# Performance work log

Hardware: AMD Instinct MI355X
Metric: run time of the kernel (lower is better)

Reference implementation:

```python
import jax, jax.numpy as jnp
import numpy as np

B, N, H, D = 2, 2048, 16, 128

def setup_inputs() -> dict:
    key = jax.random.key(0)
    kq, kk, kv = jax.random.split(key, 3)
    return {
        "query": jax.random.normal(kq, (B, N, H, D), dtype=jnp.float32),
        "key": jax.random.normal(kk, (B, N, H, D), dtype=jnp.float32),
        "value": jax.random.normal(kv, (B, N, H, D), dtype=jnp.float32),
    }

def reference(query, key, value):
    # inputs are [b, n, h, d]; module transposes to [b, h, n, d]
    q = jnp.transpose(query, (0, 2, 1, 3))  # bhnd
    k = jnp.transpose(key, (0, 2, 1, 3))    # bhmd
    v = jnp.transpose(value, (0, 2, 1, 3))  # bhmd
    # NOTE: original applies NO 1/sqrt(d) scaling
    scores = jnp.einsum('bhnd,bhmd->bhnm', q, k)
    attn = jax.nn.softmax(scores, axis=-1)
    return jnp.einsum('bhnm,bhmd->bhnd', attn, v)  # [b, h, n, d]
```

## Files before the change

kernel.cpp:

```cpp
#include <hip/hip_runtime.h>
#include <hip/hip_bf16.h>
#include <stdint.h>


constexpr int Bb = 2, Nn = 2048, Hh = 16, Dd = 128;
constexpr int ROWSTR = Hh * Dd;
constexpr size_t TEN_ELEMS = (size_t)Bb * Nn * Hh * Dd;
constexpr size_t WS_NEED = 3 * TEN_ELEMS * 2;

typedef __attribute__((ext_vector_type(8))) _Float16 f16x8;
typedef __attribute__((ext_vector_type(4))) float f32x4;

__device__ __forceinline__ unsigned short f2h(float f) {
  union { _Float16 h; unsigned short u; } v;
  v.h = (_Float16)f;
  return v.u;
}

__device__ __forceinline__ void gload_lds16(const void* g, void* l) {
  __builtin_amdgcn_global_load_lds(
      (const __attribute__((address_space(1))) unsigned int*)g,
      (__attribute__((address_space(3))) unsigned int*)l, 16, 0, 0);
}

__global__ __launch_bounds__(512) void conv_qk(
    const float* __restrict__ Q, const float* __restrict__ K,
    _Float16* __restrict__ Qf, _Float16* __restrict__ Kf) {
  size_t id = (size_t)blockIdx.x * 512 + threadIdx.x;
  const float* src;
  _Float16* dst;
  size_t e;
  if (id < TEN_ELEMS / 8) { src = Q; dst = Qf; e = id * 8; }
  else { src = K; dst = Kf; e = (id - TEN_ELEMS / 8) * 8; }
  float4 a = *(const float4*)(src + e);
  float4 b = *(const float4*)(src + e + 4);
  f16x8 t;
  t[0] = (_Float16)a.x; t[1] = (_Float16)a.y; t[2] = (_Float16)a.z; t[3] = (_Float16)a.w;
  t[4] = (_Float16)b.x; t[5] = (_Float16)b.y; t[6] = (_Float16)b.z; t[7] = (_Float16)b.w;
  *(f16x8*)(dst + e) = t;
}

__global__ __launch_bounds__(256) void conv_v(
    const float* __restrict__ V, _Float16* __restrict__ Vt) {
  __shared__ alignas(16) short T[128 * 72];
  const int tid = threadIdx.x;
  const int bid = blockIdx.x;
  const int bh = bid >> 5;
  const int n0 = (bid & 31) * 64;
  const int h = bh & 15, b = bh >> 4;
  const float* src = V + (((size_t)b * Nn + n0) * Hh + h) * Dd;
#pragma unroll
  for (int it = 0; it < 8; ++it) {
    int id = it * 256 + tid;
    int f = id & 31, n = id >> 5;
    float4 a = *(const float4*)(src + (size_t)n * ROWSTR + f * 4);
    T[(4 * f + 0) * 72 + n] = (short)f2h(a.x);
    T[(4 * f + 1) * 72 + n] = (short)f2h(a.y);
    T[(4 * f + 2) * 72 + n] = (short)f2h(a.z);
    T[(4 * f + 3) * 72 + n] = (short)f2h(a.w);
  }
  __syncthreads();
  _Float16* dst = Vt + (size_t)bh * Dd * Nn + n0;
#pragma unroll
  for (int it = 0; it < 4; ++it) {
    int cid = it * 256 + tid;
    int d = cid >> 3, nc = cid & 7;
    f16x8 v = *(const f16x8*)((const char*)T + d * 144 + nc * 16);
    *(f16x8*)(dst + (size_t)d * Nn + nc * 8) = v;
  }
}

__global__ __launch_bounds__(512, 2) void attn_f16(
    const _Float16* __restrict__ Qf, const _Float16* __restrict__ Kf,
    const _Float16* __restrict__ Vt, float* __restrict__ O) {
  __shared__ alignas(16) short LDS[98304 / 2];
  char* base = (char*)LDS;

  const int tid = threadIdx.x;
  const int wave = tid >> 6;
  const int lane = tid & 63;
  const int g = (lane >> 4) & 3;
  const int l15 = lane & 15;

  const int raw = blockIdx.x;
  const int wg = (raw & 7) * 32 + (raw >> 3);
  const int qb = wg & 7;
  const int bh = wg >> 3;
  const int h = bh & 15, b = bh >> 4;
  const int q0 = qb * 256;

  const char* K0 = (const char*)Kf + ((size_t)b * Nn * Hh + h) * 256;
  const char* Q0 = (const char*)Qf + ((size_t)b * Nn * Hh + h) * 256;
  const char* V0 = (const char*)Vt + (size_t)bh * Dd * Nn * 2;
  float* Ob = O + (size_t)bh * Nn * Dd;

  const int wq0 = q0 + wave * 32;
  f16x8 qf[2][4];
#pragma unroll
  for (int qs = 0; qs < 2; ++qs) {
    const char* qp = Q0 + (size_t)(wq0 + qs * 16 + l15) * 4096;
#pragma unroll
    for (int c = 0; c < 4; ++c)
      qf[qs][c] = *(const f16x8*)(qp + c * 64 + g * 16);
  }

  f32x4 acc[2][8];
#pragma unroll
  for (int qs = 0; qs < 2; ++qs)
#pragma unroll
    for (int dt = 0; dt < 8; ++dt) acc[qs][dt] = (f32x4){0.f, 0.f, 0.f, 0.f};
  float m_run[2][4], l_run[2][4];
#pragma unroll
  for (int qs = 0; qs < 2; ++qs)
#pragma unroll
    for (int r = 0; r < 4; ++r) { m_run[qs][r] = -INFINITY; l_run[qs][r] = 0.f; }

  char* PB = base + 65536 + wave * 4096;

  auto STAGE = [&](int bufsel, int kt) {
    const int kv0 = kt * 64;
    char* kdst = base + bufsel * 16384;
    char* vdst = base + 32768 + bufsel * 16384;
#pragma unroll
    for (int i = 0; i < 2; ++i) {
      int ob = i * 8192 + wave * 1024;
      int o = ob + lane * 16;
      int kv = o >> 8, ir = o & 255;
      gload_lds16(K0 + (size_t)(kv0 + kv) * 4096 + (ir ^ ((kv & 7) << 4)), kdst + ob);
      int d = o >> 7, ir2 = o & 127;
      gload_lds16(V0 + (size_t)d * 4096 + kv0 * 2 + (ir2 ^ ((d & 7) << 4)), vdst + ob);
    }
  };

  STAGE(0, 0);
  __syncthreads();
  int cur = 0;

  for (int kt = 0; kt < Nn / 64; ++kt) {
    if (kt < Nn / 64 - 1) STAGE(cur ^ 1, kt + 1);
    const char* KB = base + cur * 16384;
    const char* VB = base + 32768 + cur * 16384;

    f32x4 s[2][4];
#pragma unroll
    for (int qs = 0; qs < 2; ++qs)
#pragma unroll
      for (int t4 = 0; t4 < 4; ++t4) s[qs][t4] = (f32x4){0.f, 0.f, 0.f, 0.f};
#pragma unroll
    for (int t4 = 0; t4 < 4; ++t4) {
      const int row = t4 * 16 + l15;
      const int ro = row * 256;
      const int swz = (row & 7) << 4;
#pragma unroll
      for (int c = 0; c < 4; ++c) {
        f16x8 kf = *(const f16x8*)(KB + ro + ((c * 64 + g * 16) ^ swz));
        s[0][t4] = __builtin_amdgcn_mfma_f32_16x16x32_f16(qf[0][c], kf, s[0][t4], 0, 0, 0);
        s[1][t4] = __builtin_amdgcn_mfma_f32_16x16x32_f16(qf[1][c], kf, s[1][t4], 0, 0, 0);
      }
    }

#pragma unroll
    for (int qs = 0; qs < 2; ++qs) {
#pragma unroll
      for (int r = 0; r < 4; ++r) {
        float mx = fmaxf(fmaxf(s[qs][0][r], s[qs][1][r]), fmaxf(s[qs][2][r], s[qs][3][r]));
        mx = fmaxf(mx, __shfl_xor(mx, 1));
        mx = fmaxf(mx, __shfl_xor(mx, 2));
        mx = fmaxf(mx, __shfl_xor(mx, 4));
        mx = fmaxf(mx, __shfl_xor(mx, 8));
        float mn = fmaxf(m_run[qs][r], mx);
        float e = exp2f((m_run[qs][r] - mn) * 1.44269504f);
        float ps = 0.f;
#pragma unroll
        for (int t4 = 0; t4 < 4; ++t4) {
          float pv = exp2f((s[qs][t4][r] - mn) * 1.44269504f);
          s[qs][t4][r] = pv;
          ps += pv;
        }
        ps += __shfl_xor(ps, 1);
        ps += __shfl_xor(ps, 2);
        ps += __shfl_xor(ps, 4);
        ps += __shfl_xor(ps, 8);
        l_run[qs][r] = l_run[qs][r] * e + ps;
        m_run[qs][r] = mn;
#pragma unroll
        for (int dt = 0; dt < 8; ++dt) acc[qs][dt][r] *= e;
      }
#pragma unroll
      for (int t4 = 0; t4 < 4; ++t4)
#pragma unroll
        for (int r = 0; r < 4; ++r) {
          int qq = qs * 16 + 4 * g + r;
          int byte = qq * 128 + (((t4 * 16 + l15) * 2) ^ ((qq & 7) << 4));
          *(unsigned short*)(PB + byte) = f2h(s[qs][t4][r]);
        }
    }

#pragma unroll
    for (int c2 = 0; c2 < 2; ++c2) {
      f16x8 pf0 = *(const f16x8*)(PB + l15 * 128 + ((c2 * 64 + g * 16) ^ ((l15 & 7) << 4)));
      f16x8 pf1 = *(const f16x8*)(PB + (16 + l15) * 128 + ((c2 * 64 + g * 16) ^ ((l15 & 7) << 4)));
#pragma unroll
      for (int dt = 0; dt < 8; ++dt) {
        const int d = dt * 16 + l15;
        f16x8 vf = *(const f16x8*)(VB + d * 128 + ((c2 * 64 + g * 16) ^ ((d & 7) << 4)));
        acc[0][dt] = __builtin_amdgcn_mfma_f32_16x16x32_f16(pf0, vf, acc[0][dt], 0, 0, 0);
        acc[1][dt] = __builtin_amdgcn_mfma_f32_16x16x32_f16(pf1, vf, acc[1][dt], 0, 0, 0);
      }
    }
    __syncthreads();
    cur ^= 1;
  }

#pragma unroll
  for (int qs = 0; qs < 2; ++qs)
#pragma unroll
    for (int r = 0; r < 4; ++r) {
      float inv = 1.0f / l_run[qs][r];
      float* op = Ob + (size_t)(wq0 + qs * 16 + 4 * g + r) * Dd + l15;
#pragma unroll
      for (int dt = 0; dt < 8; ++dt) op[dt * 16] = acc[qs][dt][r] * inv;
    }
}

__global__ __launch_bounds__(256, 2) void attn_fwd_kernel(
    const float* __restrict__ Q, const float* __restrict__ K,
    const float* __restrict__ V, float* __restrict__ O) {
  __shared__ alignas(16) short Klds[64 * Dd];
  __shared__ alignas(16) short Vtlds[Dd * 64];
  __shared__ alignas(16) short Plds[4][16 * 64];

  const int tid = threadIdx.x;
  const int wave = tid >> 6;
  const int lane = tid & 63;
  const int g = lane >> 4;
  const int l15 = lane & 15;

  const int qb = blockIdx.x & 31;
  const int h = (blockIdx.x >> 5) & 15;
  const int b = blockIdx.x >> 9;

  const float* Qb = Q + ((size_t)b * Nn * Hh + h) * Dd;
  const float* Kb = K + ((size_t)b * Nn * Hh + h) * Dd;
  const float* Vb = V + ((size_t)b * Nn * Hh + h) * Dd;
  float* Ob = O + ((size_t)(b * Hh + h) * Nn) * Dd;

  const int qrow = qb * 64 + wave * 16 + l15;
  f16x8 qf[4];
  {
    const float* qp = Qb + (size_t)qrow * ROWSTR;
#pragma unroll
    for (int c = 0; c < 4; ++c) {
      const float* p = qp + c * 32 + g * 8;
      float4 a = *(const float4*)(p);
      float4 bb = *(const float4*)(p + 4);
      f16x8 t;
      t[0] = (_Float16)a.x;  t[1] = (_Float16)a.y;
      t[2] = (_Float16)a.z;  t[3] = (_Float16)a.w;
      t[4] = (_Float16)bb.x; t[5] = (_Float16)bb.y;
      t[6] = (_Float16)bb.z; t[7] = (_Float16)bb.w;
      qf[c] = t;
    }
  }

  f32x4 acc[8];
#pragma unroll
  for (int i = 0; i < 8; ++i) acc[i] = (f32x4){0.f, 0.f, 0.f, 0.f};
  float m_run[4], l_run[4];
#pragma unroll
  for (int r = 0; r < 4; ++r) { m_run[r] = -INFINITY; l_run[r] = 0.f; }

  char* KB = (char*)Klds;
  char* VB = (char*)Vtlds;
  char* PB = (char*)(Plds[wave]);

  for (int kt = 0; kt < Nn / 64; ++kt) {
    const int kv0 = kt * 64;
    __syncthreads();
#pragma unroll
    for (int i = 0; i < 8; ++i) {
      int id = i * 256 + tid;
      int f = id & 31;
      int kv = id >> 5;
      const float* p = Kb + (size_t)(kv0 + kv) * ROWSTR + f * 4;
      float4 a = *(const float4*)p;
      unsigned long long pk =
          (unsigned long long)f2h(a.x) | ((unsigned long long)f2h(a.y) << 16) |
          ((unsigned long long)f2h(a.z) << 32) | ((unsigned long long)f2h(a.w) << 48);
      int byte = kv * 256 + ((f * 8) ^ ((kv & 7) << 4));
      *(unsigned long long*)(KB + byte) = pk;
    }
#pragma unroll
    for (int i = 0; i < 8; ++i) {
      int id = i * 256 + tid;
      int d = id & 127;
      int kq = id >> 7;
      const float* p = Vb + (size_t)(kv0 + kq * 4) * ROWSTR + d;
      float v0 = p[0];
      float v1 = p[ROWSTR];
      float v2 = p[2 * ROWSTR];
      float v3 = p[3 * ROWSTR];
      unsigned long long pk =
          (unsigned long long)f2h(v0) | ((unsigned long long)f2h(v1) << 16) |
          ((unsigned long long)f2h(v2) << 32) | ((unsigned long long)f2h(v3) << 48);
      int byte = d * 128 + ((kq * 8) ^ ((d & 7) << 4));
      *(unsigned long long*)(VB + byte) = pk;
    }
    __syncthreads();

    f32x4 s[4];
#pragma unroll
    for (int t = 0; t < 4; ++t) {
      f32x4 cacc = (f32x4){0.f, 0.f, 0.f, 0.f};
      int row = t * 16 + l15;
#pragma unroll
      for (int c = 0; c < 4; ++c) {
        int byte = row * 256 + (((c * 64) + g * 16) ^ ((row & 7) << 4));
        f16x8 kf = *(const f16x8*)(KB + byte);
        cacc = __builtin_amdgcn_mfma_f32_16x16x32_f16(qf[c], kf, cacc, 0, 0, 0);
      }
      s[t] = cacc;
    }

#pragma unroll
    for (int r = 0; r < 4; ++r) {
      float mx = fmaxf(fmaxf(s[0][r], s[1][r]), fmaxf(s[2][r], s[3][r]));
      mx = fmaxf(mx, __shfl_xor(mx, 1));
      mx = fmaxf(mx, __shfl_xor(mx, 2));
      mx = fmaxf(mx, __shfl_xor(mx, 4));
      mx = fmaxf(mx, __shfl_xor(mx, 8));
      float mn = fmaxf(m_run[r], mx);
      float e = exp2f((m_run[r] - mn) * 1.44269504f);
      float ps = 0.f;
#pragma unroll
      for (int t = 0; t < 4; ++t) {
        float pv = exp2f((s[t][r] - mn) * 1.44269504f);
        s[t][r] = pv;
        ps += pv;
      }
      ps += __shfl_xor(ps, 1);
      ps += __shfl_xor(ps, 2);
      ps += __shfl_xor(ps, 4);
      ps += __shfl_xor(ps, 8);
      l_run[r] = l_run[r] * e + ps;
      m_run[r] = mn;
#pragma unroll
      for (int dt = 0; dt < 8; ++dt) acc[dt][r] *= e;
    }

#pragma unroll
    for (int t = 0; t < 4; ++t)
#pragma unroll
      for (int r = 0; r < 4; ++r) {
        int q = g * 4 + r;
        int kv = t * 16 + l15;
        int byte = q * 128 + ((kv * 2) ^ ((q & 7) << 4));
        *(unsigned short*)(PB + byte) = f2h(s[t][r]);
      }

#pragma unroll
    for (int c2 = 0; c2 < 2; ++c2) {
      int pbyte = l15 * 128 + (((c2 * 64) + g * 16) ^ ((l15 & 7) << 4));
      f16x8 pf = *(const f16x8*)(PB + pbyte);
#pragma unroll
      for (int dt = 0; dt < 8; ++dt) {
        int d = dt * 16 + l15;
        int vbyte = d * 128 + (((c2 * 64) + g * 16) ^ ((d & 7) << 4));
        f16x8 vf = *(const f16x8*)(VB + vbyte);
        acc[dt] = __builtin_amdgcn_mfma_f32_16x16x32_f16(pf, vf, acc[dt], 0, 0, 0);
      }
    }
  }

  const int qout = qb * 64 + wave * 16;
#pragma unroll
  for (int r = 0; r < 4; ++r) {
    float inv = 1.0f / l_run[r];
    float* op = Ob + (size_t)(qout + g * 4 + r) * Dd + l15;
#pragma unroll
    for (int dt = 0; dt < 8; ++dt) {
      op[dt * 16] = acc[dt][r] * inv;
    }
  }
}

extern "C" void kernel_launch(void* const* d_in, const int* in_sizes, int n_in,
                              void* d_out, int out_size, void* d_ws, size_t ws_size,
                              hipStream_t stream) {
  const float* Q = (const float*)d_in[0];
  const float* K = (const float*)d_in[1];
  const float* V = (const float*)d_in[2];
  float* O = (float*)d_out;

  if (ws_size >= WS_NEED) {
    _Float16* Qf = (_Float16*)d_ws;
    _Float16* Kf = Qf + TEN_ELEMS;
    _Float16* Vt = Kf + TEN_ELEMS;
    conv_qk<<<dim3(4096), 512, 0, stream>>>(Q, K, Qf, Kf);
    conv_v<<<dim3(1024), 256, 0, stream>>>(V, Vt);
    attn_f16<<<dim3(256), 512, 0, stream>>>(Qf, Kf, Vt, O);
  } else {
    attn_fwd_kernel<<<dim3(1024), 256, 0, stream>>>(Q, K, V, O);
  }
}
```

Baseline: 274.8 us.

## Rewrite attention core with 32x32 MFMA, register-resident P, and lazy rescaling

Measured after the change: 222.0 us. -19.2%, faster.

```diff
diff --git a/kernel.cpp b/kernel.cpp
--- a/kernel.cpp
+++ b/kernel.cpp
@@ -5,11 +5,13 @@
 
 constexpr int Bb = 2, Nn = 2048, Hh = 16, Dd = 128;
 constexpr int ROWSTR = Hh * Dd;
-constexpr size_t TEN_ELEMS = (size_t)Bb * Nn * Hh * Dd;
-constexpr size_t WS_NEED = 3 * TEN_ELEMS * 2;
+constexpr size_t TEN = (size_t)Bb * Nn * Hh * Dd;
+constexpr size_t WS_NEED = 2 * TEN * 2;
 
 typedef __attribute__((ext_vector_type(8))) _Float16 f16x8;
+typedef __attribute__((ext_vector_type(2))) __fp16 fp16x2;
 typedef __attribute__((ext_vector_type(4))) float f32x4;
+typedef __attribute__((ext_vector_type(16))) float f32x16;
 
 __device__ __forceinline__ unsigned short f2h(float f) {
   union { _Float16 h; unsigned short u; } v;
@@ -17,27 +19,35 @@
   return v.u;
 }
 
+__device__ __forceinline__ unsigned pk2(float a, float b) {
+  union { fp16x2 h; unsigned u; } v;
+  v.h = __builtin_amdgcn_cvt_pkrtz(a, b);
+  return v.u;
+}
+
 __device__ __forceinline__ void gload_lds16(const void* g, void* l) {
   __builtin_amdgcn_global_load_lds(
       (const __attribute__((address_space(1))) unsigned int*)g,
       (__attribute__((address_space(3))) unsigned int*)l, 16, 0, 0);
 }
 
-__global__ __launch_bounds__(512) void conv_qk(
-    const float* __restrict__ Q, const float* __restrict__ K,
-    _Float16* __restrict__ Qf, _Float16* __restrict__ Kf) {
+__device__ __forceinline__ f32x16 zero16() {
+  f32x16 z;
+#pragma unroll
+  for (int i = 0; i < 16; ++i) z[i] = 0.f;
+  return z;
+}
+
+__global__ __launch_bounds__(512) void conv_k(
+    const float* __restrict__ K, _Float16* __restrict__ Kf) {
   size_t id = (size_t)blockIdx.x * 512 + threadIdx.x;
-  const float* src;
-  _Float16* dst;
-  size_t e;
-  if (id < TEN_ELEMS / 8) { src = Q; dst = Qf; e = id * 8; }
-  else { src = K; dst = Kf; e = (id - TEN_ELEMS / 8) * 8; }
-  float4 a = *(const float4*)(src + e);
-  float4 b = *(const float4*)(src + e + 4);
+  size_t e = id * 8;
+  float4 a = *(const float4*)(K + e);
+  float4 b = *(const float4*)(K + e + 4);
   f16x8 t;
   t[0] = (_Float16)a.x; t[1] = (_Float16)a.y; t[2] = (_Float16)a.z; t[3] = (_Float16)a.w;
   t[4] = (_Float16)b.x; t[5] = (_Float16)b.y; t[6] = (_Float16)b.z; t[7] = (_Float16)b.w;
-  *(f16x8*)(dst + e) = t;
+  *(f16x8*)(Kf + e) = t;
 }
 
 __global__ __launch_bounds__(256) void conv_v(
@@ -70,69 +80,73 @@
   }
 }
 
-__global__ __launch_bounds__(512, 2) void attn_f16(
-    const _Float16* __restrict__ Qf, const _Float16* __restrict__ Kf,
+__global__ __launch_bounds__(256, 2) void attn32(
+    const float* __restrict__ Q, const _Float16* __restrict__ Kf,
     const _Float16* __restrict__ Vt, float* __restrict__ O) {
-  __shared__ alignas(16) short LDS[98304 / 2];
-  char* base = (char*)LDS;
+  __shared__ alignas(16) char base[65536];
 
   const int tid = threadIdx.x;
   const int wave = tid >> 6;
   const int lane = tid & 63;
-  const int g = (lane >> 4) & 3;
-  const int l15 = lane & 15;
+  const int l31 = lane & 31;
+  const int hi = lane >> 5;
 
   const int raw = blockIdx.x;
-  const int wg = (raw & 7) * 32 + (raw >> 3);
-  const int qb = wg & 7;
-  const int bh = wg >> 3;
+  const int wg = (raw & 7) * 64 + (raw >> 3);
+  const int qb = wg & 15;
+  const int bh = wg >> 4;
   const int h = bh & 15, b = bh >> 4;
-  const int q0 = qb * 256;
 
   const char* K0 = (const char*)Kf + ((size_t)b * Nn * Hh + h) * 256;
-  const char* Q0 = (const char*)Qf + ((size_t)b * Nn * Hh + h) * 256;
   const char* V0 = (const char*)Vt + (size_t)bh * Dd * Nn * 2;
+  const float* Q0 = Q + ((size_t)b * Nn * Hh + h) * 128;
   float* Ob = O + (size_t)bh * Nn * Dd;
 
-  const int wq0 = q0 + wave * 32;
-  f16x8 qf[2][4];
-#pragma unroll
-  for (int qs = 0; qs < 2; ++qs) {
-    const char* qp = Q0 + (size_t)(wq0 + qs * 16 + l15) * 4096;
-#pragma unroll
-    for (int c = 0; c < 4; ++c)
-      qf[qs][c] = *(const f16x8*)(qp + c * 64 + g * 16);
-  }
-
-  f32x4 acc[2][8];
-#pragma unroll
-  for (int qs = 0; qs < 2; ++qs)
-#pragma unroll
-    for (int dt = 0; dt < 8; ++dt) acc[qs][dt] = (f32x4){0.f, 0.f, 0.f, 0.f};
-  float m_run[2][4], l_run[2][4];
-#pragma unroll
-  for (int qs = 0; qs < 2; ++qs)
-#pragma unroll
-    for (int r = 0; r < 4; ++r) { m_run[qs][r] = -INFINITY; l_run[qs][r] = 0.f; }
-
-  char* PB = base + 65536 + wave * 4096;
-
-  auto STAGE = [&](int bufsel, int kt) {
-    const int kv0 = kt * 64;
-    char* kdst = base + bufsel * 16384;
-    char* vdst = base + 32768 + bufsel * 16384;
-#pragma unroll
-    for (int i = 0; i < 2; ++i) {
-      int ob = i * 8192 + wave * 1024;
+  const int wq0 = qb * 128 + wave * 32;
+  const int kswz = (l31 & 15) << 4;
+  const int vswz = (l31 & 7) << 4;
+
+  auto STAGE = [&](int buf, int kt) {
+    const size_t kv0 = (size_t)kt * 64;
+    char* kd = base + buf * 16384;
+    char* vd = base + 32768 + buf * 16384;
+    const char* ks = K0 + kv0 * 4096;
+    const char* vs = V0 + kv0 * 2;
+#pragma unroll
+    for (int i = 0; i < 4; ++i) {
+      int ob = i * 4096 + wave * 1024;
       int o = ob + lane * 16;
-      int kv = o >> 8, ir = o & 255;
-      gload_lds16(K0 + (size_t)(kv0 + kv) * 4096 + (ir ^ ((kv & 7) << 4)), kdst + ob);
-      int d = o >> 7, ir2 = o & 127;
-      gload_lds16(V0 + (size_t)d * 4096 + kv0 * 2 + (ir2 ^ ((d & 7) << 4)), vdst + ob);
+      int kv = o >> 8, ck = o & 255;
+      gload_lds16(ks + (size_t)kv * 4096 + (ck ^ ((kv & 15) << 4)), kd + ob);
+      int d = o >> 7, cv = o & 127;
+      gload_lds16(vs + (size_t)d * 4096 + (cv ^ ((d & 7) << 4)), vd + ob);
     }
   };
 
   STAGE(0, 0);
+
+  f16x8 qf[8];
+  {
+    const float* qp = Q0 + (size_t)(wq0 + l31) * ROWSTR;
+#pragma unroll
+    for (int c = 0; c < 8; ++c) {
+      const float* p = qp + c * 16 + hi * 8;
+      float4 a = *(const float4*)p;
+      float4 bb = *(const float4*)(p + 4);
+      f16x8 t;
+      t[0] = (_Float16)a.x;  t[1] = (_Float16)a.y;
+      t[2] = (_Float16)a.z;  t[3] = (_Float16)a.w;
+      t[4] = (_Float16)bb.x; t[5] = (_Float16)bb.y;
+      t[6] = (_Float16)bb.z; t[7] = (_Float16)bb.w;
+      qf[c] = t;
+    }
+  }
+
+  f32x16 acc[4];
+#pragma unroll
+  for (int dt = 0; dt < 4; ++dt) acc[dt] = zero16();
+  float m_run = -INFINITY, l_run = 0.f;
+
   __syncthreads();
   int cur = 0;
 
@@ -141,85 +155,89 @@
     const char* KB = base + cur * 16384;
     const char* VB = base + 32768 + cur * 16384;
 
-    f32x4 s[2][4];
-#pragma unroll
-    for (int qs = 0; qs < 2; ++qs)
-#pragma unroll
-      for (int t4 = 0; t4 < 4; ++t4) s[qs][t4] = (f32x4){0.f, 0.f, 0.f, 0.f};
-#pragma unroll
-    for (int t4 = 0; t4 < 4; ++t4) {
-      const int row = t4 * 16 + l15;
-      const int ro = row * 256;
-      const int swz = (row & 7) << 4;
-#pragma unroll
-      for (int c = 0; c < 4; ++c) {
-        f16x8 kf = *(const f16x8*)(KB + ro + ((c * 64 + g * 16) ^ swz));
-        s[0][t4] = __builtin_amdgcn_mfma_f32_16x16x32_f16(qf[0][c], kf, s[0][t4], 0, 0, 0);
-        s[1][t4] = __builtin_amdgcn_mfma_f32_16x16x32_f16(qf[1][c], kf, s[1][t4], 0, 0, 0);
-      }
-    }
-
-#pragma unroll
-    for (int qs = 0; qs < 2; ++qs) {
-#pragma unroll
-      for (int r = 0; r < 4; ++r) {
-        float mx = fmaxf(fmaxf(s[qs][0][r], s[qs][1][r]), fmaxf(s[qs][2][r], s[qs][3][r]));
-        mx = fmaxf(mx, __shfl_xor(mx, 1));
-        mx = fmaxf(mx, __shfl_xor(mx, 2));
-        mx = fmaxf(mx, __shfl_xor(mx, 4));
-        mx = fmaxf(mx, __shfl_xor(mx, 8));
-        float mn = fmaxf(m_run[qs][r], mx);
-        float e = exp2f((m_run[qs][r] - mn) * 1.44269504f);
-        float ps = 0.f;
-#pragma unroll
-        for (int t4 = 0; t4 < 4; ++t4) {
-          float pv = exp2f((s[qs][t4][r] - mn) * 1.44269504f);
-          s[qs][t4][r] = pv;
-          ps += pv;
-        }
-        ps += __shfl_xor(ps, 1);
-        ps += __shfl_xor(ps, 2);
-        ps += __shfl_xor(ps, 4);
-        ps += __shfl_xor(ps, 8);
-        l_run[qs][r] = l_run[qs][r] * e + ps;
-        m_run[qs][r] = mn;
-#pragma unroll
-        for (int dt = 0; dt < 8; ++dt) acc[qs][dt][r] *= e;
-      }
-#pragma unroll
-      for (int t4 = 0; t4 < 4; ++t4)
-#pragma unroll
-        for (int r = 0; r < 4; ++r) {
-          int qq = qs * 16 + 4 * g + r;
-          int byte = qq * 128 + (((t4 * 16 + l15) * 2) ^ ((qq & 7) << 4));
-          *(unsigned short*)(PB + byte) = f2h(s[qs][t4][r]);
-        }
-    }
-
-#pragma unroll
-    for (int c2 = 0; c2 < 2; ++c2) {
-      f16x8 pf0 = *(const f16x8*)(PB + l15 * 128 + ((c2 * 64 + g * 16) ^ ((l15 & 7) << 4)));
-      f16x8 pf1 = *(const f16x8*)(PB + (16 + l15) * 128 + ((c2 * 64 + g * 16) ^ ((l15 & 7) << 4)));
-#pragma unroll
-      for (int dt = 0; dt < 8; ++dt) {
-        const int d = dt * 16 + l15;
-        f16x8 vf = *(const f16x8*)(VB + d * 128 + ((c2 * 64 + g * 16) ^ ((d & 7) << 4)));
-        acc[0][dt] = __builtin_amdgcn_mfma_f32_16x16x32_f16(pf0, vf, acc[0][dt], 0, 0, 0);
-        acc[1][dt] = __builtin_amdgcn_mfma_f32_16x16x32_f16(pf1, vf, acc[1][dt], 0, 0, 0);
-      }
-    }
+    f32x16 s[2];
+    s[0] = zero16();
+    s[1] = zero16();
+#pragma unroll
+    for (int c = 0; c < 8; ++c) {
+      const int colc = 32 * c + 16 * hi;
+      f16x8 k0 = *(const f16x8*)(KB + l31 * 256 + (colc ^ kswz));
+      f16x8 k1 = *(const f16x8*)(KB + (l31 + 32) * 256 + (colc ^ kswz));
+      s[0] = __builtin_amdgcn_mfma_f32_32x32x16_f16(k0, qf[c], s[0], 0, 0, 0);
+      s[1] = __builtin_amdgcn_mfma_f32_32x32x16_f16(k1, qf[c], s[1], 0, 0, 0);
+    }
+
+    float mx = s[0][0];
+#pragma unroll
+    for (int r = 1; r < 16; ++r) mx = fmaxf(mx, s[0][r]);
+#pragma unroll
+    for (int r = 0; r < 16; ++r) mx = fmaxf(mx, s[1][r]);
+    mx = fmaxf(mx, __shfl_xor(mx, 32));
+
+    if (!__all(mx <= m_run + 8.0f)) {
+      float mn = fmaxf(m_run, mx);
+      float e = exp2f((m_run - mn) * 1.44269504f);
+      l_run *= e;
+#pragma unroll
+      for (int dt = 0; dt < 4; ++dt)
+#pragma unroll
+        for (int r = 0; r < 16; ++r) acc[dt][r] *= e;
+      m_run = mn;
+    }
+    float ps = 0.f;
+#pragma unroll
+    for (int sub = 0; sub < 2; ++sub)
+#pragma unroll
+      for (int r = 0; r < 16; ++r) {
+        float pv = exp2f((s[sub][r] - m_run) * 1.44269504f);
+        s[sub][r] = pv;
+        ps += pv;
+      }
+    ps += __shfl_xor(ps, 32);
+    l_run += ps;
+
+    f16x8 pa[4];
+#pragma unroll
+    for (int ks = 0; ks < 4; ++ks) {
+      const int sub = ks >> 1, kb = ks & 1;
+      float v0 = s[sub][8 * kb + 0], v1 = s[sub][8 * kb + 1];
+      float v2 = s[sub][8 * kb + 2], v3 = s[sub][8 * kb + 3];
+      float v4 = s[sub][8 * kb + 4], v5 = s[sub][8 * kb + 5];
+      float v6 = s[sub][8 * kb + 6], v7 = s[sub][8 * kb + 7];
+      unsigned uA0 = pk2(v0, v1), uA1 = pk2(v2, v3);
+      unsigned uB0 = pk2(v4, v5), uB1 = pk2(v6, v7);
+      unsigned r0 = (unsigned)__shfl_xor((int)(hi ? uA0 : uB0), 32);
+      unsigned r1 = (unsigned)__shfl_xor((int)(hi ? uA1 : uB1), 32);
+      union { unsigned u[4]; f16x8 v; } t;
+      t.u[0] = hi ? r0 : uA0;
+      t.u[1] = hi ? r1 : uA1;
+      t.u[2] = hi ? uB0 : r0;
+      t.u[3] = hi ? uB1 : r1;
+      pa[ks] = t.v;
+    }
+
+#pragma unroll
+    for (int dt = 0; dt < 4; ++dt) {
+      const char* vrow = VB + (32 * dt + l31) * 128;
+#pragma unroll
+      for (int ks = 0; ks < 4; ++ks) {
+        f16x8 vf = *(const f16x8*)(vrow + ((32 * ks + 16 * hi) ^ vswz));
+        acc[dt] = __builtin_amdgcn_mfma_f32_32x32x16_f16(vf, pa[ks], acc[dt], 0, 0, 0);
+      }
+    }
+
     __syncthreads();
     cur ^= 1;
   }
 
-#pragma unroll
-  for (int qs = 0; qs < 2; ++qs)
-#pragma unroll
-    for (int r = 0; r < 4; ++r) {
-      float inv = 1.0f / l_run[qs][r];
-      float* op = Ob + (size_t)(wq0 + qs * 16 + 4 * g + r) * Dd + l15;
-#pragma unroll
-      for (int dt = 0; dt < 8; ++dt) op[dt * 16] = acc[qs][dt][r] * inv;
+  const float invl = 1.0f / l_run;
+  float* orow = Ob + (size_t)(wq0 + l31) * Dd;
+#pragma unroll
+  for (int dt = 0; dt < 4; ++dt)
+#pragma unroll
+    for (int r = 0; r < 16; ++r) {
+      int d = 32 * dt + (r & 3) + 8 * (r >> 2) + 4 * hi;
+      orow[d] = acc[dt][r] * invl;
     }
 }
 
@@ -393,12 +411,11 @@
   float* O = (float*)d_out;
 
   if (ws_size >= WS_NEED) {
-    _Float16* Qf = (_Float16*)d_ws;
-    _Float16* Kf = Qf + TEN_ELEMS;
-    _Float16* Vt = Kf + TEN_ELEMS;
-    conv_qk<<<dim3(4096), 512, 0, stream>>>(Q, K, Qf, Kf);
+    _Float16* Kf = (_Float16*)d_ws;
+    _Float16* Vt = Kf + TEN;
+    conv_k<<<dim3(TEN / 8 / 512), 512, 0, stream>>>(K, Kf);
     conv_v<<<dim3(1024), 256, 0, stream>>>(V, Vt);
-    attn_f16<<<dim3(256), 512, 0, stream>>>(Qf, Kf, Vt, O);
+    attn32<<<dim3(512), 256, 0, stream>>>(Q, Kf, Vt, O);
   } else {
     attn_fwd_kernel<<<dim3(1024), 256, 0, stream>>>(Q, K, V, O);
   }
```
